# Optimization experiments

Measured on AMD Instinct MI355X. Metric: run time of the kernel, lower is better.

## Reference

```python
import jax, jax.numpy as jnp
import numpy as np

S, B, H = 4096, 32, 512

def setup_inputs() -> dict:
    key = jax.random.key(0)
    k1, k2, k3, k4, k5, k6 = jax.random.split(key, 6)
    sc = 1.0 / np.sqrt(H)
    return {
        "hidden_states": jax.random.normal(k1, (S, B, H), dtype=jnp.float32),
        "Wq": jax.random.normal(k2, (H, H), dtype=jnp.float32) * sc,
        "bq": jax.random.normal(k3, (H,), dtype=jnp.float32) * sc,
        "Wk": jax.random.normal(k4, (H, H), dtype=jnp.float32) * sc,
        "bk": jax.random.normal(k5, (H,), dtype=jnp.float32) * sc,
        "lengths": jax.random.randint(k6, (B,), 1, S + 1, dtype=jnp.int64),
    }

def reference(hidden_states, Wq, bq, Wk, bk, lengths):
    # hidden_states: [S, B, H] (time-first, as in the torch module)
    # query projection then mean over time -> [B, H]
    q = jnp.mean(hidden_states @ Wq.T + bq, axis=0)
    # key: tanh(linear) -> [S, B, H], then batch-first [B, S, H]
    key = jnp.tanh(hidden_states @ Wk.T + bk)
    key_bsh = jnp.transpose(key, (1, 0, 2))
    # attention scores: [B, S]
    scores = jnp.einsum("bsh,bh->bs", key_bsh, q)
    # length mask: positions >= length get -10000 (additive, as in torch code)
    pos = jnp.arange(scores.shape[1])[None, :]
    mask = (pos >= lengths[:, None]).astype(scores.dtype) * -10000.0
    probs = jax.nn.softmax(scores + mask, axis=-1)
    # weighted sum of keys -> [B, H]
    return jnp.einsum("bs,bsh->bh", probs, key_bsh)
```

## Files before the change

kernel.cpp:

```cpp
#include <hip/hip_runtime.h>
#include <hip/hip_fp16.h>

#define S_LEN 4096
#define B_N   32
#define H_N   512
#define BH    (B_N * H_N)
#define CROWS 64
#define NCH   (S_LEN / CROWS)

typedef __attribute__((ext_vector_type(8))) short bf16x8;
typedef __attribute__((ext_vector_type(4))) float f32x4;
typedef __attribute__((ext_vector_type(4))) unsigned short us4;

__device__ __forceinline__ unsigned short f2bf(float x) {
    union { float f; unsigned u; } c; c.f = x;
    unsigned r = c.u + 0x7fffu + ((c.u >> 16) & 1u);
    return (unsigned short)(r >> 16);
}

__global__ __launch_bounds__(256) void wkfrag_kernel(const float* __restrict__ Wk,
                                                     unsigned short* __restrict__ WbF) {
    int g = blockIdx.x * 256 + threadIdx.x;
    int lane = g & 63;
    int n    = (g >> 6) & 7;
    int ks   = (g >> 9) & 15;
    int wn   = g >> 13;
    int col = wn * 128 + n * 16 + (lane & 15);
    int k   = ks * 32 + (lane >> 4) * 8;
    const float* src = Wk + (size_t)col * H_N + k;
    float4 v0 = *(const float4*)(src);
    float4 v1 = *(const float4*)(src + 4);
    us4 a = {f2bf(v0.x), f2bf(v0.y), f2bf(v0.z), f2bf(v0.w)};
    us4 b = {f2bf(v1.x), f2bf(v1.y), f2bf(v1.z), f2bf(v1.w)};
    *(us4*)(WbF + (size_t)g * 8)     = a;
    *(us4*)(WbF + (size_t)g * 8 + 4) = b;
}

__global__ __launch_bounds__(256) void hsum_kernel(const float* __restrict__ hs,
                                                   float* __restrict__ hsum) {
    int col = (blockIdx.x * 256 + threadIdx.x) * 4;
    size_t s0 = (size_t)blockIdx.y * 128;
    float4 acc = {0.f, 0.f, 0.f, 0.f};
    #pragma unroll 8
    for (int i = 0; i < 128; ++i) {
        float4 v = *(const float4*)(hs + (s0 + i) * BH + col);
        acc.x += v.x; acc.y += v.y; acc.z += v.z; acc.w += v.w;
    }
    atomicAdd(&hsum[col],     acc.x);
    atomicAdd(&hsum[col + 1], acc.y);
    atomicAdd(&hsum[col + 2], acc.z);
    atomicAdd(&hsum[col + 3], acc.w);
}

__global__ __launch_bounds__(256) void q_kernel(const float* __restrict__ hsum,
                                                const float* __restrict__ Wq,
                                                const float* __restrict__ bq,
                                                float* __restrict__ q) {
    int b = blockIdx.x, t = threadIdx.x;
    __shared__ float hrow[H_N];
    hrow[t]       = hsum[b * H_N + t]       * (1.f / S_LEN);
    hrow[t + 256] = hsum[b * H_N + t + 256] * (1.f / S_LEN);
    __syncthreads();
    for (int h = t; h < H_N; h += 256) {
        const float* wrow = Wq + (size_t)h * H_N;
        float acc = 0.f;
        #pragma unroll 8
        for (int k = 0; k < H_N; ++k) acc = fmaf(hrow[k], wrow[k], acc);
        q[b * H_N + h] = acc + bq[h];
    }
}

__global__ __launch_bounds__(512, 4) void fused_kernel(
    const float* __restrict__ hs, const unsigned short* __restrict__ WbF,
    const float* __restrict__ bk, const float* __restrict__ qv,
    const int* __restrict__ lengths,
    float* __restrict__ pm, float* __restrict__ pl, float* __restrict__ po)
{
    int blk = blockIdx.x;
    int b = blk & 31;
    int chunk = blk >> 5;
    int s0 = chunk * CROWS;
    int t = threadIdx.x;

    int len = lengths[b];
    if (s0 >= len) {
        po[((size_t)b * NCH + chunk) * H_N + t] = 0.f;
        if (t == 0) { pm[b * NCH + chunk] = -1e30f; pl[b * NCH + chunk] = 0.f; }
        return;
    }

    int lane = t & 63, wv = t >> 6;
    int l15 = lane & 15, lg = lane >> 4;
    int wm = wv >> 2, wn = wv & 3;

    __shared__ __align__(16) unsigned short A_s[CROWS * H_N];
    __shared__ float q_s[H_N];
    __shared__ float bk_s[H_N];
    __shared__ float scp[4][CROWS];
    __shared__ float score_s[CROWS];
    __shared__ float p_s[CROWS];

    q_s[t]  = qv[b * H_N + t];
    bk_s[t] = bk[t];

    const float* hb = hs + ((size_t)s0 * B_N + b) * H_N;
    int kq  = t & 127;
    int r0l = t >> 7;
    #pragma unroll 8
    for (int j = 0; j < 16; ++j) {
        int row = r0l + 4 * j;
        float4 v = *(const float4*)(hb + (size_t)row * BH + kq * 4);
        us4 u = {f2bf(v.x), f2bf(v.y), f2bf(v.z), f2bf(v.w)};
        *(us4*)((char*)A_s + row * 1024 + ((kq * 8) ^ ((row & 7) << 4))) = u;
    }
    __syncthreads();

    const unsigned short* wbF = WbF + (size_t)wn * 65536 + lane * 8;
    const char* Ab = (const char*)A_s + (wm * 32 + l15) * 1024;
    int axor = (l15 & 7) << 4;

    f32x4 acc[2][8];
    #pragma unroll
    for (int m = 0; m < 2; ++m)
        #pragma unroll
        for (int n = 0; n < 8; ++n) acc[m][n] = (f32x4){0.f, 0.f, 0.f, 0.f};

    #pragma unroll
    for (int ks = 0; ks < 16; ++ks) {
        const unsigned short* wk = wbF + ks * 4096;
        bf16x8 b0 = *(const bf16x8*)(wk + 0 * 512);
        bf16x8 b1 = *(const bf16x8*)(wk + 1 * 512);
        bf16x8 b2 = *(const bf16x8*)(wk + 2 * 512);
        bf16x8 b3 = *(const bf16x8*)(wk + 3 * 512);
        bf16x8 b4 = *(const bf16x8*)(wk + 4 * 512);
        bf16x8 b5 = *(const bf16x8*)(wk + 5 * 512);
        bf16x8 b6 = *(const bf16x8*)(wk + 6 * 512);
        bf16x8 b7 = *(const bf16x8*)(wk + 7 * 512);
        int off = (ks * 64 + lg * 16) ^ axor;
        bf16x8 a0 = *(const bf16x8*)(Ab + off);
        bf16x8 a1 = *(const bf16x8*)(Ab + 16 * 1024 + off);
        __builtin_amdgcn_s_setprio(1);
        acc[0][0] = __builtin_amdgcn_mfma_f32_16x16x32_bf16(a0, b0, acc[0][0], 0, 0, 0);
        acc[1][0] = __builtin_amdgcn_mfma_f32_16x16x32_bf16(a1, b0, acc[1][0], 0, 0, 0);
        acc[0][1] = __builtin_amdgcn_mfma_f32_16x16x32_bf16(a0, b1, acc[0][1], 0, 0, 0);
        acc[1][1] = __builtin_amdgcn_mfma_f32_16x16x32_bf16(a1, b1, acc[1][1], 0, 0, 0);
        acc[0][2] = __builtin_amdgcn_mfma_f32_16x16x32_bf16(a0, b2, acc[0][2], 0, 0, 0);
        acc[1][2] = __builtin_amdgcn_mfma_f32_16x16x32_bf16(a1, b2, acc[1][2], 0, 0, 0);
        acc[0][3] = __builtin_amdgcn_mfma_f32_16x16x32_bf16(a0, b3, acc[0][3], 0, 0, 0);
        acc[1][3] = __builtin_amdgcn_mfma_f32_16x16x32_bf16(a1, b3, acc[1][3], 0, 0, 0);
        acc[0][4] = __builtin_amdgcn_mfma_f32_16x16x32_bf16(a0, b4, acc[0][4], 0, 0, 0);
        acc[1][4] = __builtin_amdgcn_mfma_f32_16x16x32_bf16(a1, b4, acc[1][4], 0, 0, 0);
        acc[0][5] = __builtin_amdgcn_mfma_f32_16x16x32_bf16(a0, b5, acc[0][5], 0, 0, 0);
        acc[1][5] = __builtin_amdgcn_mfma_f32_16x16x32_bf16(a1, b5, acc[1][5], 0, 0, 0);
        acc[0][6] = __builtin_amdgcn_mfma_f32_16x16x32_bf16(a0, b6, acc[0][6], 0, 0, 0);
        acc[1][6] = __builtin_amdgcn_mfma_f32_16x16x32_bf16(a1, b6, acc[1][6], 0, 0, 0);
        acc[0][7] = __builtin_amdgcn_mfma_f32_16x16x32_bf16(a0, b7, acc[0][7], 0, 0, 0);
        acc[1][7] = __builtin_amdgcn_mfma_f32_16x16x32_bf16(a1, b7, acc[1][7], 0, 0, 0);
        __builtin_amdgcn_s_setprio(0);
    }

    float sp[2][4] = {{0,0,0,0},{0,0,0,0}};
    #pragma unroll
    for (int m = 0; m < 2; ++m)
        #pragma unroll
        for (int n = 0; n < 8; ++n) {
            int c = wn * 128 + n * 16 + l15;
            float bkv = bk_s[c], qc = q_s[c];
            #pragma unroll
            for (int i = 0; i < 4; ++i) {
                float z = acc[m][n][i] + bkv;
                float e = __expf(2.f * z);
                float kv = 1.f - 2.f / (e + 1.f);
                acc[m][n][i] = kv;
                sp[m][i] = fmaf(kv, qc, sp[m][i]);
            }
        }
    #pragma unroll
    for (int m = 0; m < 2; ++m)
        #pragma unroll
        for (int i = 0; i < 4; ++i) {
            float v = sp[m][i];
            v += __shfl_xor(v, 1); v += __shfl_xor(v, 2);
            v += __shfl_xor(v, 4); v += __shfl_xor(v, 8);
            if (l15 == 0) scp[wn][wm * 32 + m * 16 + lg * 4 + i] = v;
        }
    __syncthreads();

    if (t < CROWS) {
        float sc = scp[0][t] + scp[1][t] + scp[2][t] + scp[3][t];
        if (s0 + t >= len) sc -= 10000.f;
        score_s[t] = sc;
    }
    __syncthreads();
    float mx = -1e30f;
    #pragma unroll 8
    for (int r = 0; r < CROWS; ++r) mx = fmaxf(mx, score_s[r]);
    if (t < CROWS) p_s[t] = __expf(score_s[t] - mx);
    __syncthreads();

    float* opart = (float*)A_s;
    float o8[8] = {0,0,0,0,0,0,0,0};
    #pragma unroll
    for (int m = 0; m < 2; ++m)
        #pragma unroll
        for (int i = 0; i < 4; ++i) {
            float p = p_s[wm * 32 + m * 16 + lg * 4 + i];
            #pragma unroll
            for (int n = 0; n < 8; ++n) o8[n] = fmaf(p, acc[m][n][i], o8[n]);
        }
    int slice = wm * 4 + lg;
    #pragma unroll
    for (int n = 0; n < 8; ++n) opart[slice * H_N + wn * 128 + n * 16 + l15] = o8[n];
    __syncthreads();

    {
        float o = 0.f;
        #pragma unroll
        for (int s = 0; s < 8; ++s) o += opart[s * H_N + t];
        po[((size_t)b * NCH + chunk) * H_N + t] = o;
    }
    if (t == 0) {
        float l = 0.f;
        #pragma unroll 8
        for (int r = 0; r < CROWS; ++r) l += p_s[r];
        pm[b * NCH + chunk] = mx;
        pl[b * NCH + chunk] = l;
    }
}

__global__ __launch_bounds__(256) void combine_kernel(
    const float* __restrict__ pm, const float* __restrict__ pl,
    const float* __restrict__ po, float* __restrict__ out)
{
    int b = blockIdx.x, t = threadIdx.x;
    float M = -1e30f;
    for (int c = 0; c < NCH; ++c) M = fmaxf(M, pm[b * NCH + c]);
    float den = 0.f, n0 = 0.f, n1 = 0.f;
    for (int c = 0; c < NCH; ++c) {
        float w = __expf(pm[b * NCH + c] - M);
        den = fmaf(w, pl[b * NCH + c], den);
        const float* op = po + (size_t)(b * NCH + c) * H_N;
        n0 = fmaf(w, op[t], n0);
        n1 = fmaf(w, op[t + 256], n1);
    }
    out[b * H_N + t]       = n0 / den;
    out[b * H_N + t + 256] = n1 / den;
}

extern "C" void kernel_launch(void* const* d_in, const int* in_sizes, int n_in,
                              void* d_out, int out_size, void* d_ws, size_t ws_size,
                              hipStream_t stream) {
    const float* hs      = (const float*)d_in[0];
    const float* Wq      = (const float*)d_in[1];
    const float* bq      = (const float*)d_in[2];
    const float* Wk      = (const float*)d_in[3];
    const float* bk      = (const float*)d_in[4];
    const int*   lengths = (const int*)d_in[5];
    float* out = (float*)d_out;

    float* ws   = (float*)d_ws;
    float* hsum = ws;
    float* qv   = hsum + BH;
    float* pm   = qv + BH;
    float* pl   = pm + B_N * NCH;
    float* po   = pl + B_N * NCH;
    unsigned short* WbF = (unsigned short*)(po + (size_t)B_N * NCH * H_N);

    hipMemsetAsync(hsum, 0, BH * sizeof(float), stream);
    hipLaunchKernelGGL(wkfrag_kernel, dim3(128), dim3(256), 0, stream, Wk, WbF);
    hipLaunchKernelGGL(hsum_kernel, dim3(BH / 1024, S_LEN / 128), dim3(256), 0, stream, hs, hsum);
    hipLaunchKernelGGL(q_kernel, dim3(B_N), dim3(256), 0, stream, hsum, Wq, bq, qv);
    hipLaunchKernelGGL(fused_kernel, dim3(B_N * NCH), dim3(512), 0, stream,
                       hs, WbF, bk, qv, lengths, pm, pl, po);
    hipLaunchKernelGGL(combine_kernel, dim3(B_N), dim3(256), 0, stream, pm, pl, po, out);
}
```

Before: 222.1 us.

## Fuse bf16 tile conversion into hsum pass and stream tiles via global_load_lds

The column-sum kernel is replaced by a per-(batch, chunk) prep kernel. While it reads hidden_states for the mean, it also writes a pre-swizzled bf16 copy of each 64-row tile to the workspace, skipping chunks past the sequence length. The fused kernel no longer reads fp32 hidden_states and converts them. Instead it copies the ready bf16 tile straight into LDS with global_load_lds, so the fp32 activations are read once instead of twice. In exchange there is an extra bf16 write and read of up to half the input size, more workspace, and a different hsum access pattern with more atomics per column.

New measurement: 244.1 us. 9.9% more time.

```diff
diff --git a/kernel.cpp b/kernel.cpp
--- a/kernel.cpp
+++ b/kernel.cpp
@@ -16,6 +16,12 @@
     union { float f; unsigned u; } c; c.f = x;
     unsigned r = c.u + 0x7fffu + ((c.u >> 16) & 1u);
     return (unsigned short)(r >> 16);
+}
+
+__device__ __forceinline__ void gload_lds16(const void* g, void* l) {
+    __builtin_amdgcn_global_load_lds(
+        (__attribute__((address_space(1))) void*)g,
+        (__attribute__((address_space(3))) void*)l, 16, 0, 0);
 }
 
 __global__ __launch_bounds__(256) void wkfrag_kernel(const float* __restrict__ Wk,
@@ -36,20 +42,34 @@
     *(us4*)(WbF + (size_t)g * 8 + 4) = b;
 }
 
-__global__ __launch_bounds__(256) void hsum_kernel(const float* __restrict__ hs,
-                                                   float* __restrict__ hsum) {
-    int col = (blockIdx.x * 256 + threadIdx.x) * 4;
-    size_t s0 = (size_t)blockIdx.y * 128;
-    float4 acc = {0.f, 0.f, 0.f, 0.f};
+__global__ __launch_bounds__(256) void prep_kernel(const float* __restrict__ hs,
+                                                   float* __restrict__ hsum,
+                                                   unsigned short* __restrict__ AT,
+                                                   const int* __restrict__ lengths) {
+    int blk = blockIdx.x;
+    int b = blk & 31, chunk = blk >> 5;
+    int s0 = chunk * CROWS;
+    bool active = (s0 < lengths[b]);
+    int t = threadIdx.x;
+    int kq = t & 127, r0 = t >> 7;
+    const float* hb = hs + ((size_t)s0 * B_N + b) * H_N + kq * 4;
+    char* tile = (char*)(AT + (size_t)blk * (CROWS * H_N));
+    float4 sum = {0.f, 0.f, 0.f, 0.f};
     #pragma unroll 8
-    for (int i = 0; i < 128; ++i) {
-        float4 v = *(const float4*)(hs + (s0 + i) * BH + col);
-        acc.x += v.x; acc.y += v.y; acc.z += v.z; acc.w += v.w;
-    }
-    atomicAdd(&hsum[col],     acc.x);
-    atomicAdd(&hsum[col + 1], acc.y);
-    atomicAdd(&hsum[col + 2], acc.z);
-    atomicAdd(&hsum[col + 3], acc.w);
+    for (int j = 0; j < 32; ++j) {
+        int row = r0 + 2 * j;
+        float4 v = *(const float4*)(hb + (size_t)row * BH);
+        sum.x += v.x; sum.y += v.y; sum.z += v.z; sum.w += v.w;
+        if (active) {
+            us4 u = {f2bf(v.x), f2bf(v.y), f2bf(v.z), f2bf(v.w)};
+            *(us4*)(tile + row * 1024 + ((kq * 8) ^ ((row & 7) << 4))) = u;
+        }
+    }
+    int col = b * H_N + kq * 4;
+    atomicAdd(&hsum[col],     sum.x);
+    atomicAdd(&hsum[col + 1], sum.y);
+    atomicAdd(&hsum[col + 2], sum.z);
+    atomicAdd(&hsum[col + 3], sum.w);
 }
 
 __global__ __launch_bounds__(256) void q_kernel(const float* __restrict__ hsum,
@@ -71,7 +91,7 @@
 }
 
 __global__ __launch_bounds__(512, 4) void fused_kernel(
-    const float* __restrict__ hs, const unsigned short* __restrict__ WbF,
+    const unsigned short* __restrict__ AT, const unsigned short* __restrict__ WbF,
     const float* __restrict__ bk, const float* __restrict__ qv,
     const int* __restrict__ lengths,
     float* __restrict__ pm, float* __restrict__ pl, float* __restrict__ po)
@@ -100,19 +120,17 @@
     __shared__ float score_s[CROWS];
     __shared__ float p_s[CROWS];
 
+    const char* tsrc = (const char*)(AT + (size_t)blk * (CROWS * H_N));
+    {
+        int wbase = wv * 8192;
+        #pragma unroll
+        for (int j = 0; j < 8; ++j) {
+            int off = wbase + j * 1024;
+            gload_lds16(tsrc + off + lane * 16, (char*)A_s + off);
+        }
+    }
     q_s[t]  = qv[b * H_N + t];
     bk_s[t] = bk[t];
-
-    const float* hb = hs + ((size_t)s0 * B_N + b) * H_N;
-    int kq  = t & 127;
-    int r0l = t >> 7;
-    #pragma unroll 8
-    for (int j = 0; j < 16; ++j) {
-        int row = r0l + 4 * j;
-        float4 v = *(const float4*)(hb + (size_t)row * BH + kq * 4);
-        us4 u = {f2bf(v.x), f2bf(v.y), f2bf(v.z), f2bf(v.w)};
-        *(us4*)((char*)A_s + row * 1024 + ((kq * 8) ^ ((row & 7) << 4))) = u;
-    }
     __syncthreads();
 
     const unsigned short* wbF = WbF + (size_t)wn * 65536 + lane * 8;
@@ -265,12 +283,13 @@
     float* pl   = pm + B_N * NCH;
     float* po   = pl + B_N * NCH;
     unsigned short* WbF = (unsigned short*)(po + (size_t)B_N * NCH * H_N);
+    unsigned short* AT  = WbF + (size_t)H_N * H_N;
 
     hipMemsetAsync(hsum, 0, BH * sizeof(float), stream);
     hipLaunchKernelGGL(wkfrag_kernel, dim3(128), dim3(256), 0, stream, Wk, WbF);
-    hipLaunchKernelGGL(hsum_kernel, dim3(BH / 1024, S_LEN / 128), dim3(256), 0, stream, hs, hsum);
+    hipLaunchKernelGGL(prep_kernel, dim3(B_N * NCH), dim3(256), 0, stream, hs, hsum, AT, lengths);
     hipLaunchKernelGGL(q_kernel, dim3(B_N), dim3(256), 0, stream, hsum, Wq, bq, qv);
     hipLaunchKernelGGL(fused_kernel, dim3(B_N * NCH), dim3(512), 0, stream,
-                       hs, WbF, bk, qv, lengths, pm, pl, po);
+                       AT, WbF, bk, qv, lengths, pm, pl, po);
     hipLaunchKernelGGL(combine_kernel, dim3(B_N), dim3(256), 0, stream, pm, pl, po, out);
 }
```
